# Performance work log

Hardware: AMD Instinct MI355X
Metric: run time of the kernel (lower is better)

## Reference

```python
import jax, jax.numpy as jnp
import numpy as np

N_NODES = 50000
N_EDGES = 800000
NODE_IN = 10
EDGE_IN = 7
H = 128
N_LAYERS = 6
OUT_DIM = 3


def setup_inputs() -> dict:
    key = jax.random.key(0)
    ks = jax.random.split(key, 32)
    s = 0.05
    inp = {
        "x": jax.random.normal(ks[0], (N_NODES, NODE_IN), jnp.float32),
        "edge_attr": jax.random.normal(ks[1], (N_EDGES, EDGE_IN), jnp.float32),
        "edge_index": jax.random.randint(ks[2], (2, N_EDGES), 0, N_NODES, jnp.int32),
        "bc_disp": jax.random.uniform(ks[3], (N_NODES, 1), jnp.float32),
        "bc_rot": jax.random.uniform(ks[4], (N_NODES, 1), jnp.float32),
        # node encoder: MLP(10, [H], H)
        "ne_w1": jax.random.normal(ks[5], (NODE_IN, H), jnp.float32) * s,
        "ne_b1": jnp.zeros((H,), jnp.float32),
        "ne_w2": jax.random.normal(ks[6], (H, H), jnp.float32) * s,
        "ne_b2": jnp.zeros((H,), jnp.float32),
        # edge encoder: MLP(7, [H], H)
        "ee_w1": jax.random.normal(ks[7], (EDGE_IN, H), jnp.float32) * s,
        "ee_b1": jnp.zeros((H,), jnp.float32),
        "ee_w2": jax.random.normal(ks[8], (H, H), jnp.float32) * s,
        "ee_b2": jnp.zeros((H,), jnp.float32),
        # 6 GraphNetworkLayers: edge model (3H -> H), node model (2H -> H)
        "mp_ew": jax.random.normal(ks[9], (N_LAYERS, 3 * H, H), jnp.float32) * s,
        "mp_eb": jnp.zeros((N_LAYERS, H), jnp.float32),
        "mp_nw": jax.random.normal(ks[10], (N_LAYERS, 2 * H, H), jnp.float32) * s,
        "mp_nb": jnp.zeros((N_LAYERS, H), jnp.float32),
        "d_w1": jax.random.normal(ks[11], (H, H), jnp.float32) * s,
        "d_b1": jnp.zeros((H,), jnp.float32),
        "d_w2": jax.random.normal(ks[12], (H, 64), jnp.float32) * s,
        "d_b2": jnp.zeros((64,), jnp.float32),
        "d_w3": jax.random.normal(ks[13], (64, OUT_DIM), jnp.float32) * (s * 5.0),
        "d_b3": jnp.full((OUT_DIM,), 0.5, jnp.float32),
    }
    return inp


def reference(x, edge_attr, edge_index, bc_disp, bc_rot,
              ne_w1, ne_b1, ne_w2, ne_b2,
              ee_w1, ee_b1, ee_w2, ee_b2,
              mp_ew, mp_eb, mp_nw, mp_nb,
              d_w1, d_b1, d_w2, d_b2, d_w3, d_b3):
    # encode nodes and edges (Linear -> ReLU -> Linear)
    h = jax.nn.relu(x @ ne_w1 + ne_b1) @ ne_w2 + ne_b2            # [N, H]
    e = jax.nn.relu(edge_attr @ ee_w1 + ee_b1) @ ee_w2 + ee_b2    # [E, H]
    src = edge_index[0]
    dst = edge_index[1]
    # 6 residual message-passing layers: gather -> edge MLP -> scatter-add -> node MLP
    for l in range(N_LAYERS):
        msg_in = jnp.concatenate([h[src], h[dst], e], axis=-1)    # [E, 3H]
        msg = jax.nn.relu(msg_in @ mp_ew[l] + mp_eb[l])           # [E, H]
        agg = jax.ops.segment_sum(msg, dst, num_segments=N_NODES)  # [N, H] (aggr='add')
        upd = jax.nn.relu(jnp.concatenate([h, agg], axis=-1) @ mp_nw[l] + mp_nb[l])
        h = h + upd                                               # residual
    # decode: Linear -> ReLU -> Linear -> ReLU -> Linear
    z = jax.nn.relu(h @ d_w1 + d_b1)
    z = jax.nn.relu(z @ d_w2 + d_b2)
    pred = z @ d_w3 + d_b3                                        # [N, 3]
    # hard boundary conditions
    pred = jnp.concatenate([pred[:, 0:2] * (1.0 - bc_disp),
                            pred[:, 2:3] * (1.0 - bc_rot)], axis=-1)
    return pred
```

## Files before the change

### kernel.cpp

```cpp
#include <hip/hip_runtime.h>
#include <hip/hip_bf16.h>

#define NN 50000
#define NE 800000
#define H 128

typedef __hip_bfloat16 bf16;
typedef __attribute__((ext_vector_type(8))) short short8v;
typedef __attribute__((ext_vector_type(4))) float f32x4;

static __device__ __forceinline__ unsigned short f2bf_bits(float x) {
  union { __hip_bfloat16 b; unsigned short u; } cv;
  cv.b = __float2bfloat16(x);
  return cv.u;
}

__global__ __launch_bounds__(256) void zero_counts_kernel(int* __restrict__ counts) {
  int i = blockIdx.x * 256 + threadIdx.x;
  if (i < NN) counts[i] = 0;
}

__global__ __launch_bounds__(256) void hist_kernel(const int* __restrict__ dstI,
                                                   int* __restrict__ counts) {
  int e = blockIdx.x * 256 + threadIdx.x;
  if (e < NE) atomicAdd(&counts[dstI[e]], 1);
}

__global__ __launch_bounds__(256) void scan_kernel(const int* __restrict__ counts,
                                                   int* __restrict__ cursor) {
  __shared__ int sdata[256];
  __shared__ int sbase;
  const int t = threadIdx.x;
  if (t == 0) sbase = 0;
  __syncthreads();
  for (int c0 = 0; c0 < NN; c0 += 256) {
    int i = c0 + t;
    int v = (i < NN) ? counts[i] : 0;
    sdata[t] = v;
    __syncthreads();
    #pragma unroll
    for (int off = 1; off < 256; off <<= 1) {
      int x = (t >= off) ? sdata[t - off] : 0;
      __syncthreads();
      sdata[t] += x;
      __syncthreads();
    }
    if (i < NN) cursor[i] = sbase + sdata[t] - v;
    __syncthreads();
    if (t == 255) sbase += sdata[255];
    __syncthreads();
  }
}

__global__ __launch_bounds__(256) void scatter_kernel(
    const float* __restrict__ ea, const int* __restrict__ srcI, const int* __restrict__ dstI,
    int* __restrict__ cursor, bf16* __restrict__ eap,
    int* __restrict__ srcp, int* __restrict__ dstp) {
  int e = blockIdx.x * 256 + threadIdx.x;
  if (e >= NE) return;
  int d = dstI[e];
  int pos = atomicAdd(&cursor[d], 1);
  srcp[pos] = srcI[e];
  dstp[pos] = d;
  #pragma unroll
  for (int k = 0; k < 7; ++k) eap[(size_t)pos * 7 + k] = __float2bfloat16(ea[(size_t)e * 7 + k]);
}

__global__ __launch_bounds__(256) void fuse_w3_kernel(
    const float* __restrict__ ee_w2, const float* __restrict__ ee_b2,
    const float* __restrict__ mp_ew, const float* __restrict__ mp_eb,
    float* __restrict__ W3p, float* __restrict__ c3)
{
  const int l = blockIdx.x >> 3;
  const int cc = (blockIdx.x & 7) * 16;
  __shared__ float sA[H * H];
  __shared__ float sB[H * 16];
  const float* W3 = mp_ew + (size_t)l * 384 * H + 256 * H;
  for (int i = threadIdx.x; i < H * H; i += 256) sA[i] = ee_w2[i];
  for (int i = threadIdx.x; i < H * 16; i += 256) {
    int k = i >> 4, j = i & 15;
    sB[i] = W3[k * H + cc + j];
  }
  __syncthreads();
  float* out = W3p + (size_t)l * H * H;
  for (int i = threadIdx.x; i < H * 16; i += 256) {
    int r = i >> 4, j = i & 15;
    float acc = 0.f;
    #pragma unroll 8
    for (int k = 0; k < H; ++k) acc += sA[r * H + k] * sB[k * 16 + j];
    out[r * H + cc + j] = acc;
  }
  if (threadIdx.x < 16) {
    int j = threadIdx.x;
    float acc = mp_eb[l * H + cc + j];
    for (int k = 0; k < H; ++k) acc += ee_b2[k] * sB[k * 16 + j];
    c3[l * H + cc + j] = acc;
  }
}

__global__ __launch_bounds__(256) void repack_w_kernel(
    const float* __restrict__ src0, size_t lstride, bf16* __restrict__ dst0, int K)
{
  const int l = blockIdx.x;
  const float* src = src0 + (size_t)l * lstride;
  bf16* dst = dst0 + (size_t)l * K * 128;
  const int nkk = K / 32;
  const int nslots = 8 * nkk * 64;
  for (int idx = threadIdx.x; idx < nslots; idx += 256) {
    int ng = idx / (nkk * 64);
    int rem = idx % (nkk * 64);
    int kk = rem / 64, ln = rem % 64;
    #pragma unroll
    for (int j = 0; j < 8; ++j) {
      int k = kk * 32 + ((ln >> 4) * 8) + j;
      int col = ng * 16 + (ln & 15);
      dst[(size_t)idx * 8 + j] = __float2bfloat16(src[(size_t)k * 128 + col]);
    }
  }
}

__global__ __launch_bounds__(256) void node_encoder_kernel(
    const float* __restrict__ in,
    const float* __restrict__ w1, const float* __restrict__ b1,
    const float* __restrict__ w2, const float* __restrict__ b2,
    float* __restrict__ out, int nrows)
{
  __shared__ float sw1[10 * H];
  __shared__ float sw2[H * H];
  __shared__ float sb1[H];
  __shared__ float sb2[H];
  __shared__ float sin_[8][10];
  __shared__ float st[8][H];

  for (int i = threadIdx.x; i < 10 * H; i += 256) sw1[i] = w1[i];
  for (int i = threadIdx.x; i < H * H; i += 256) sw2[i] = w2[i];
  if (threadIdx.x < H) { sb1[threadIdx.x] = b1[threadIdx.x]; sb2[threadIdx.x] = b2[threadIdx.x]; }
  __syncthreads();

  const int c = threadIdx.x & 127;
  const int hf = threadIdx.x >> 7;

  for (long long r0 = (long long)blockIdx.x * 8; r0 < nrows; r0 += (long long)gridDim.x * 8) {
    if (threadIdx.x < 80) {
      int j = threadIdx.x / 10, k = threadIdx.x % 10;
      long long r = r0 + j;
      sin_[j][k] = (r < nrows) ? in[r * 10 + k] : 0.f;
    }
    __syncthreads();
    #pragma unroll
    for (int t = 0; t < 4; ++t) {
      int idx = threadIdx.x + t * 256;
      int j = idx >> 7, k = idx & 127;
      float acc = sb1[k];
      #pragma unroll
      for (int i = 0; i < 10; ++i) acc += sin_[j][i] * sw1[i * H + k];
      st[j][k] = fmaxf(acc, 0.f);
    }
    __syncthreads();
    float a0 = sb2[c], a1 = a0, a2 = a0, a3 = a0;
    #pragma unroll 4
    for (int k4 = 0; k4 < H; k4 += 4) {
      float w0 = sw2[(k4 + 0) * H + c];
      float w1v = sw2[(k4 + 1) * H + c];
      float w2v = sw2[(k4 + 2) * H + c];
      float w3v = sw2[(k4 + 3) * H + c];
      float4 s0 = *(const float4*)&st[hf * 4 + 0][k4];
      float4 s1 = *(const float4*)&st[hf * 4 + 1][k4];
      float4 s2 = *(const float4*)&st[hf * 4 + 2][k4];
      float4 s3 = *(const float4*)&st[hf * 4 + 3][k4];
      a0 += s0.x * w0 + s0.y * w1v + s0.z * w2v + s0.w * w3v;
      a1 += s1.x * w0 + s1.y * w1v + s1.z * w2v + s1.w * w3v;
      a2 += s2.x * w0 + s2.y * w1v + s2.z * w2v + s2.w * w3v;
      a3 += s3.x * w0 + s3.y * w1v + s3.z * w2v + s3.w * w3v;
    }
    float accs[4] = {a0, a1, a2, a3};
    #pragma unroll
    for (int j = 0; j < 4; ++j) {
      long long r = r0 + hf * 4 + j;
      if (r < nrows) out[r * H + c] = accs[j];
    }
    __syncthreads();
  }
}

__global__ __launch_bounds__(512) void node_AB_kernel(
    const float* __restrict__ h, const float* __restrict__ W1f, const float* __restrict__ W2f,
    bf16* __restrict__ A, bf16* __restrict__ B, float* __restrict__ agg, int nrows)
{
  __shared__ float sw1[H * H];
  __shared__ float sw2[H * H];
  __shared__ float sh[16][H];
  for (int i = threadIdx.x; i < H * H; i += 512) { sw1[i] = W1f[i]; sw2[i] = W2f[i]; }
  __syncthreads();
  const int c = threadIdx.x & 127;
  const int q = threadIdx.x >> 7;
  for (long long r0 = (long long)blockIdx.x * 16; r0 < nrows; r0 += (long long)gridDim.x * 16) {
    #pragma unroll
    for (int t = 0; t < 4; ++t) {
      int idx = threadIdx.x + t * 512;
      int j = idx >> 7, k = idx & 127;
      long long r = r0 + j;
      sh[j][k] = (r < nrows) ? h[r * H + k] : 0.f;
    }
    __syncthreads();
    float aA[4] = {0, 0, 0, 0}, aB[4] = {0, 0, 0, 0};
    #pragma unroll 2
    for (int k4 = 0; k4 < H; k4 += 4) {
      float w10 = sw1[(k4 + 0) * H + c], w11 = sw1[(k4 + 1) * H + c];
      float w12 = sw1[(k4 + 2) * H + c], w13 = sw1[(k4 + 3) * H + c];
      float w20 = sw2[(k4 + 0) * H + c], w21 = sw2[(k4 + 1) * H + c];
      float w22 = sw2[(k4 + 2) * H + c], w23 = sw2[(k4 + 3) * H + c];
      #pragma unroll
      for (int j = 0; j < 4; ++j) {
        float4 s = *(const float4*)&sh[q * 4 + j][k4];
        aA[j] += s.x * w10 + s.y * w11 + s.z * w12 + s.w * w13;
        aB[j] += s.x * w20 + s.y * w21 + s.z * w22 + s.w * w23;
      }
    }
    #pragma unroll
    for (int j = 0; j < 4; ++j) {
      long long r = r0 + q * 4 + j;
      if (r < nrows) {
        A[r * H + c] = __float2bfloat16(aA[j]);
        B[r * H + c] = __float2bfloat16(aB[j]);
        agg[r * H + c] = 0.f;
      }
    }
    __syncthreads();
  }
}

__global__ __launch_bounds__(512) void edge_mfma_scatter(
    const bf16* __restrict__ eap,
    const int* __restrict__ srcp, const int* __restrict__ dstp,
    const bf16* __restrict__ A, const bf16* __restrict__ B,
    const float* __restrict__ ew1, const float* __restrict__ eb1,
    const bf16* __restrict__ W3b, const float* __restrict__ c3,
    float* __restrict__ agg, int nE)
{
  __shared__ unsigned short seaP[64][40];
  __shared__ int didx[64];
  __shared__ unsigned int shid[64 * 64];
  __shared__ bf16 sAld[64][136];

  const int t = threadIdx.x;
  const int lane = t & 63;
  const int wid = t >> 6;
  const int hm = wid >> 2;
  const int colbase = (wid & 3) * 32;

  for (int i = t; i < 64 * 40; i += 512) ((unsigned short*)seaP)[i] = 0;

  short8v bfrag[2][4];
  float c3v[2];
  #pragma unroll
  for (int n = 0; n < 2; ++n) {
    c3v[n] = c3[colbase + n * 16 + (lane & 15)];
    int ng = (colbase >> 4) + n;
    #pragma unroll
    for (int kk = 0; kk < 4; ++kk) {
      const bf16* p = W3b + ((size_t)(ng * 4 + kk) * 64 + lane) * 8;
      bfrag[n][kk] = *(const short8v*)p;
    }
  }
  short8v bew[2];
  float eb1v[2];
  #pragma unroll
  for (int n = 0; n < 2; ++n) {
    int col = colbase + n * 16 + (lane & 15);
    eb1v[n] = eb1[col];
    #pragma unroll
    for (int j = 0; j < 8; ++j) {
      int k = (lane >> 4) * 8 + j;
      bew[n][j] = (short)((k < 7) ? f2bf_bits(ew1[k * H + col]) : 0);
    }
  }
  __syncthreads();

  const long long stride = (long long)gridDim.x * 64;
  const int elA0 = t >> 4;
  const int elA1 = 32 + (t >> 4);
  const int segA = (t & 15) * 8;

  unsigned short pf_ea = 0;
  int     pf_d = 0;
  short8v pf_A0, pf_A1;
  long long e0 = (long long)blockIdx.x * 64;
  if (e0 < nE) {
    if (t < 448) pf_ea = ((const unsigned short*)eap)[e0 * 7 + t];
    if (t < 64)  pf_d = dstp[e0 + t];
    int s0 = srcp[e0 + elA0];
    pf_A0 = *(const short8v*)&A[(size_t)s0 * H + segA];
    int s1 = srcp[e0 + elA1];
    pf_A1 = *(const short8v*)&A[(size_t)s1 * H + segA];
  }

  for (; e0 < nE; e0 += stride) {
    if (t < 448) seaP[t / 7][t % 7] = pf_ea;
    if (t < 64)  didx[t] = pf_d;
    *(short8v*)&sAld[elA0][segA] = pf_A0;
    *(short8v*)&sAld[elA1][segA] = pf_A1;
    __syncthreads();

    long long e1 = e0 + stride;
    if (e1 < nE) {
      if (t < 448) pf_ea = ((const unsigned short*)eap)[e1 * 7 + t];
      if (t < 64)  pf_d = dstp[e1 + t];
      int s0 = srcp[e1 + elA0];
      pf_A0 = *(const short8v*)&A[(size_t)s0 * H + segA];
      int s1 = srcp[e1 + elA1];
      pf_A1 = *(const short8v*)&A[(size_t)s1 * H + segA];
    }

    {
      f32x4 h1[2][2];
      const f32x4 z = {0.f, 0.f, 0.f, 0.f};
      h1[0][0] = z; h1[0][1] = z; h1[1][0] = z; h1[1][1] = z;
      #pragma unroll
      for (int m = 0; m < 2; ++m) {
        int row = hm * 32 + m * 16 + (lane & 15);
        short8v afrag = *(const short8v*)((const char*)seaP + row * 80 + (lane >> 4) * 16);
        h1[m][0] = __builtin_amdgcn_mfma_f32_16x16x32_bf16(afrag, bew[0], h1[m][0], 0, 0, 0);
        h1[m][1] = __builtin_amdgcn_mfma_f32_16x16x32_bf16(afrag, bew[1], h1[m][1], 0, 0, 0);
      }
      #pragma unroll
      for (int m = 0; m < 2; ++m) {
        #pragma unroll
        for (int r = 0; r < 4; ++r) {
          int row = hm * 32 + m * 16 + (lane >> 4) * 4 + r;
          #pragma unroll
          for (int n = 0; n < 2; ++n) {
            int col = colbase + n * 16 + (lane & 15);
            float v = fmaxf(h1[m][n][r] + eb1v[n], 0.f);
            int off = (row * 256 + col * 2) ^ ((row & 7) << 4);
            *(unsigned short*)((char*)shid + off) = f2bf_bits(v);
          }
        }
      }
    }
    __syncthreads();

    f32x4 acc[2][2];
    const f32x4 z = {0.f, 0.f, 0.f, 0.f};
    acc[0][0] = z; acc[0][1] = z; acc[1][0] = z; acc[1][1] = z;
    #pragma unroll
    for (int m = 0; m < 2; ++m) {
      #pragma unroll
      for (int kk = 0; kk < 4; ++kk) {
        int row = hm * 32 + m * 16 + (lane & 15);
        int off = (row * 256 + kk * 64 + (lane >> 4) * 16) ^ ((row & 7) << 4);
        short8v afrag = *(const short8v*)((const char*)shid + off);
        acc[m][0] = __builtin_amdgcn_mfma_f32_16x16x32_bf16(afrag, bfrag[0][kk], acc[m][0], 0, 0, 0);
        acc[m][1] = __builtin_amdgcn_mfma_f32_16x16x32_bf16(afrag, bfrag[1][kk], acc[m][1], 0, 0, 0);
      }
    }

    const int col0 = colbase + (lane & 15);
    const int col1 = col0 + 16;
    #pragma unroll
    for (int m = 0; m < 2; ++m) {
      float vs0 = 0.f, vs1 = 0.f;
      float b0 = 0.f, b1 = 0.f;
      int dprev = -1;
      #pragma unroll
      for (int r = 0; r < 4; ++r) {
        int el = hm * 32 + m * 16 + (lane >> 4) * 4 + r;
        int d = didx[el];
        if (d != dprev) {
          if (dprev >= 0) {
            atomicAdd(&agg[(size_t)dprev * H + col0], vs0);
            atomicAdd(&agg[(size_t)dprev * H + col1], vs1);
          }
          vs0 = 0.f; vs1 = 0.f;
          b0 = __bfloat162float(B[(size_t)d * H + col0]);
          b1 = __bfloat162float(B[(size_t)d * H + col1]);
          dprev = d;
        }
        float a0v = __bfloat162float(sAld[el][col0]);
        float a1v = __bfloat162float(sAld[el][col1]);
        vs0 += fmaxf(acc[m][0][r] + c3v[0] + a0v + b0, 0.f);
        vs1 += fmaxf(acc[m][1][r] + c3v[1] + a1v + b1, 0.f);
      }
      atomicAdd(&agg[(size_t)dprev * H + col0], vs0);
      atomicAdd(&agg[(size_t)dprev * H + col1], vs1);
    }
    __syncthreads();
  }
}

template<int DO_AB>
__global__ __launch_bounds__(256) void fused_update_kernel(
    float* __restrict__ h, const float* __restrict__ aggin,
    const bf16* __restrict__ Wnb, const float* __restrict__ nb,
    const bf16* __restrict__ W1b, const bf16* __restrict__ W2b,
    bf16* __restrict__ A, bf16* __restrict__ B, float* __restrict__ aggz,
    int nrows)
{
  __shared__ unsigned int sKw[32 * 128];
  unsigned short* shnew = (unsigned short*)sKw;

  const int t = threadIdx.x;
  const int lane = t & 63;
  const int wid = t >> 6;
  const int colbase = wid * 32;

  short8v bU[2][8];
  float nbv[2];
  #pragma unroll
  for (int n = 0; n < 2; ++n) {
    int ng = wid * 2 + n;
    nbv[n] = nb[colbase + n * 16 + (lane & 15)];
    #pragma unroll
    for (int kk = 0; kk < 8; ++kk)
      bU[n][kk] = *(const short8v*)(Wnb + ((size_t)(ng * 8 + kk) * 64 + lane) * 8);
  }

  const int ntiles = (nrows + 31) / 32;
  for (int tile = blockIdx.x; tile < ntiles; tile += gridDim.x) {
    const int r0 = tile * 32;
    #pragma unroll
    for (int i = 0; i < 16; ++i) {
      int w = t + i * 256;
      int row = w >> 7, k2 = w & 127;
      int r = r0 + row;
      float v0 = 0.f, v1 = 0.f;
      if (r < nrows) {
        if (k2 < 64) { float2 p = *(const float2*)&h[(size_t)r * H + 2 * k2]; v0 = p.x; v1 = p.y; }
        else         { float2 p = *(const float2*)&aggin[(size_t)r * H + 2 * k2 - 128]; v0 = p.x; v1 = p.y; }
      }
      unsigned int wrd = (unsigned int)f2bf_bits(v0) | ((unsigned int)f2bf_bits(v1) << 16);
      sKw[((w * 4) ^ ((row & 7) << 4)) >> 2] = wrd;
    }
    __syncthreads();

    f32x4 acc[2][2];
    const f32x4 z = {0.f, 0.f, 0.f, 0.f};
    acc[0][0] = z; acc[0][1] = z; acc[1][0] = z; acc[1][1] = z;
    #pragma unroll
    for (int kk = 0; kk < 8; ++kk) {
      #pragma unroll
      for (int m = 0; m < 2; ++m) {
        int row = m * 16 + (lane & 15);
        int off = (row * 512 + kk * 64 + (lane >> 4) * 16) ^ ((row & 7) << 4);
        short8v afrag = *(const short8v*)((const char*)sKw + off);
        acc[m][0] = __builtin_amdgcn_mfma_f32_16x16x32_bf16(afrag, bU[0][kk], acc[m][0], 0, 0, 0);
        acc[m][1] = __builtin_amdgcn_mfma_f32_16x16x32_bf16(afrag, bU[1][kk], acc[m][1], 0, 0, 0);
      }
    }
    __syncthreads();

    #pragma unroll
    for (int m = 0; m < 2; ++m) {
      #pragma unroll
      for (int r = 0; r < 4; ++r) {
        int row = m * 16 + (lane >> 4) * 4 + r;
        int grow = r0 + row;
        #pragma unroll
        for (int n = 0; n < 2; ++n) {
          int col = colbase + n * 16 + (lane & 15);
          float u = fmaxf(acc[m][n][r] + nbv[n], 0.f);
          float hold = (grow < nrows) ? h[(size_t)grow * H + col] : 0.f;
          float hn = hold + u;
          if (grow < nrows) h[(size_t)grow * H + col] = hn;
          if (DO_AB) {
            int i16 = (row * 128 + col) ^ ((row & 7) << 3);
            shnew[i16] = f2bf_bits(hn);
          }
        }
      }
    }

    if (DO_AB) {
      __syncthreads();
      short8v bA[2][4], bB[2][4];
      #pragma unroll
      for (int n = 0; n < 2; ++n) {
        int ng = wid * 2 + n;
        #pragma unroll
        for (int kk = 0; kk < 4; ++kk) {
          bA[n][kk] = *(const short8v*)(W1b + ((size_t)(ng * 4 + kk) * 64 + lane) * 8);
          bB[n][kk] = *(const short8v*)(W2b + ((size_t)(ng * 4 + kk) * 64 + lane) * 8);
        }
      }
      f32x4 aA[2][2], aB2[2][2];
      aA[0][0] = z; aA[0][1] = z; aA[1][0] = z; aA[1][1] = z;
      aB2[0][0] = z; aB2[0][1] = z; aB2[1][0] = z; aB2[1][1] = z;
      #pragma unroll
      for (int kk = 0; kk < 4; ++kk) {
        #pragma unroll
        for (int m = 0; m < 2; ++m) {
          int row = m * 16 + (lane & 15);
          int off = (row * 256 + kk * 64 + (lane >> 4) * 16) ^ ((row & 7) << 4);
          short8v afrag = *(const short8v*)((const char*)shnew + off);
          aA[m][0] = __builtin_amdgcn_mfma_f32_16x16x32_bf16(afrag, bA[0][kk], aA[m][0], 0, 0, 0);
          aA[m][1] = __builtin_amdgcn_mfma_f32_16x16x32_bf16(afrag, bA[1][kk], aA[m][1], 0, 0, 0);
          aB2[m][0] = __builtin_amdgcn_mfma_f32_16x16x32_bf16(afrag, bB[0][kk], aB2[m][0], 0, 0, 0);
          aB2[m][1] = __builtin_amdgcn_mfma_f32_16x16x32_bf16(afrag, bB[1][kk], aB2[m][1], 0, 0, 0);
        }
      }
      #pragma unroll
      for (int m = 0; m < 2; ++m) {
        #pragma unroll
        for (int r = 0; r < 4; ++r) {
          int row = m * 16 + (lane >> 4) * 4 + r;
          int grow = r0 + row;
          if (grow < nrows) {
            #pragma unroll
            for (int n = 0; n < 2; ++n) {
              int col = colbase + n * 16 + (lane & 15);
              A[(size_t)grow * H + col] = __float2bfloat16(aA[m][n][r]);
              B[(size_t)grow * H + col] = __float2bfloat16(aB2[m][n][r]);
              aggz[(size_t)grow * H + col] = 0.f;
            }
          }
        }
      }
    }
    __syncthreads();
  }
}

__global__ __launch_bounds__(512) void decoder_kernel(
    const float* __restrict__ h,
    const float* __restrict__ w1, const float* __restrict__ b1,
    const float* __restrict__ w2, const float* __restrict__ b2,
    const float* __restrict__ w3, const float* __restrict__ b3,
    const float* __restrict__ bcd, const float* __restrict__ bcr,
    float* __restrict__ out, int nrows)
{
  __shared__ float sw1[H * H];
  __shared__ float sw2[H * 64];
  __shared__ float sw3[64 * 3];
  __shared__ float sb1[H], sb2[64], sb3[3];
  __shared__ float sh[16][H], st1[16][H], st2[16][64];
  for (int i = threadIdx.x; i < H * H; i += 512) sw1[i] = w1[i];
  for (int i = threadIdx.x; i < H * 64; i += 512) sw2[i] = w2[i];
  if (threadIdx.x < 64 * 3) sw3[threadIdx.x] = w3[threadIdx.x];
  if (threadIdx.x < H) sb1[threadIdx.x] = b1[threadIdx.x];
  if (threadIdx.x < 64) sb2[threadIdx.x] = b2[threadIdx.x];
  if (threadIdx.x < 3) sb3[threadIdx.x] = b3[threadIdx.x];
  __syncthreads();
  for (long long r0 = (long long)blockIdx.x * 16; r0 < nrows; r0 += (long long)gridDim.x * 16) {
    #pragma unroll
    for (int t = 0; t < 4; ++t) {
      int idx = threadIdx.x + t * 512;
      int j = idx >> 7, k = idx & 127;
      long long r = r0 + j;
      sh[j][k] = (r < nrows) ? h[r * H + k] : 0.f;
    }
    __syncthreads();
    #pragma unroll
    for (int t = 0; t < 4; ++t) {
      int idx = threadIdx.x + t * 512;
      int j = idx >> 7, k = idx & 127;
      float acc = sb1[k];
      #pragma unroll 8
      for (int i = 0; i < H; ++i) acc += sh[j][i] * sw1[i * H + k];
      st1[j][k] = fmaxf(acc, 0.f);
    }
    __syncthreads();
    #pragma unroll
    for (int t = 0; t < 2; ++t) {
      int idx = threadIdx.x + t * 512;
      int j = idx >> 6, k = idx & 63;
      float acc = sb2[k];
      #pragma unroll 8
      for (int i = 0; i < H; ++i) acc += st1[j][i] * sw2[i * 64 + k];
      st2[j][k] = fmaxf(acc, 0.f);
    }
    __syncthreads();
    if (threadIdx.x < 48) {
      int j = threadIdx.x / 3, o = threadIdx.x % 3;
      float acc = sb3[o];
      #pragma unroll 8
      for (int i = 0; i < 64; ++i) acc += st2[j][i] * sw3[i * 3 + o];
      long long r = r0 + j;
      if (r < nrows) {
        float m = (o < 2) ? (1.f - bcd[r]) : (1.f - bcr[r]);
        out[r * 3 + o] = acc * m;
      }
    }
    __syncthreads();
  }
}

extern "C" void kernel_launch(void* const* d_in, const int* in_sizes, int n_in,
                              void* d_out, int out_size, void* d_ws, size_t ws_size,
                              hipStream_t stream) {
  const float* x     = (const float*)d_in[0];
  const float* ea    = (const float*)d_in[1];
  const int*   eidx  = (const int*)d_in[2];
  const float* bcd   = (const float*)d_in[3];
  const float* bcr   = (const float*)d_in[4];
  const float* ne_w1 = (const float*)d_in[5];
  const float* ne_b1 = (const float*)d_in[6];
  const float* ne_w2 = (const float*)d_in[7];
  const float* ne_b2 = (const float*)d_in[8];
  const float* ee_w1 = (const float*)d_in[9];
  const float* ee_b1 = (const float*)d_in[10];
  const float* ee_w2 = (const float*)d_in[11];
  const float* ee_b2 = (const float*)d_in[12];
  const float* mp_ew = (const float*)d_in[13];
  const float* mp_eb = (const float*)d_in[14];
  const float* mp_nw = (const float*)d_in[15];
  const float* mp_nb = (const float*)d_in[16];
  const float* d_w1  = (const float*)d_in[17];
  const float* d_b1  = (const float*)d_in[18];
  const float* d_w2  = (const float*)d_in[19];
  const float* d_b2  = (const float*)d_in[20];
  const float* d_w3  = (const float*)d_in[21];
  const float* d_b3  = (const float*)d_in[22];

  const int* srcI = eidx;
  const int* dstI = eidx + NE;

  char* wsp = (char*)d_ws;
  float* h    = (float*)wsp; wsp += (size_t)NN * H * 4;
  float* agg  = (float*)wsp; wsp += (size_t)NN * H * 4;
  bf16*  A    = (bf16*)wsp;  wsp += (size_t)NN * H * 2;
  bf16*  B    = (bf16*)wsp;  wsp += (size_t)NN * H * 2;
  bf16*  eap  = (bf16*)wsp;  wsp += (size_t)NE * 7 * 2;
  int*   srcp = (int*)wsp;   wsp += (size_t)NE * 4;
  int*   dstp = (int*)wsp;   wsp += (size_t)NE * 4;
  bf16*  W3b  = (bf16*)wsp;  wsp += (size_t)6 * H * H * 2;
  bf16*  Wnb  = (bf16*)wsp;  wsp += (size_t)6 * 256 * H * 2;
  bf16*  W1b  = (bf16*)wsp;  wsp += (size_t)6 * H * H * 2;
  bf16*  W2b  = (bf16*)wsp;  wsp += (size_t)6 * H * H * 2;
  float* c3   = (float*)wsp; wsp += (size_t)6 * H * 4;
  int*   counts = (int*)A;
  int*   cursor = (int*)A + NN;
  float* W3p    = agg;

  zero_counts_kernel<<<(NN + 255) / 256, 256, 0, stream>>>(counts);
  hist_kernel<<<(NE + 255) / 256, 256, 0, stream>>>(dstI, counts);
  scan_kernel<<<1, 256, 0, stream>>>(counts, cursor);
  scatter_kernel<<<(NE + 255) / 256, 256, 0, stream>>>(ea, srcI, dstI, cursor, eap, srcp, dstp);

  fuse_w3_kernel<<<48, 256, 0, stream>>>(ee_w2, ee_b2, mp_ew, mp_eb, W3p, c3);
  repack_w_kernel<<<6, 256, 0, stream>>>(W3p, (size_t)H * H, W3b, 128);
  repack_w_kernel<<<6, 256, 0, stream>>>(mp_nw, (size_t)256 * H, Wnb, 256);
  repack_w_kernel<<<6, 256, 0, stream>>>(mp_ew, (size_t)384 * H, W1b, 128);
  repack_w_kernel<<<6, 256, 0, stream>>>(mp_ew + 128 * H, (size_t)384 * H, W2b, 128);

  node_encoder_kernel<<<2048, 256, 0, stream>>>(x, ne_w1, ne_b1, ne_w2, ne_b2, h, NN);
  node_AB_kernel<<<1024, 512, 0, stream>>>(h, mp_ew, mp_ew + 128 * H, A, B, agg, NN);

  for (int l = 0; l < 6; ++l) {
    edge_mfma_scatter<<<6250, 512, 0, stream>>>(eap, srcp, dstp, A, B, ee_w1, ee_b1,
                                                W3b + (size_t)l * H * H, c3 + l * H, agg, NE);
    if (l < 5) {
      fused_update_kernel<1><<<1563, 256, 0, stream>>>(
          h, agg, Wnb + (size_t)l * 256 * H, mp_nb + l * H,
          W1b + (size_t)(l + 1) * H * H, W2b + (size_t)(l + 1) * H * H,
          A, B, agg, NN);
    } else {
      fused_update_kernel<0><<<1563, 256, 0, stream>>>(
          h, agg, Wnb + (size_t)l * 256 * H, mp_nb + l * H,
          nullptr, nullptr, nullptr, nullptr, nullptr, NN);
    }
  }

  decoder_kernel<<<1024, 512, 0, stream>>>(h, d_w1, d_b1, d_w2, d_b2, d_w3, d_b3,
                                           bcd, bcr, (float*)d_out, NN);
}
```

Measured before the change: 2.810 ms.

## Assign destination segments to owning blocks and replace the serial scan

The edge kernel now gives each 64-edge block ownership of the destination segments that start within its range, extending into the next 64 edges to finish a boundary segment. It accumulates up to 16 owned destinations in shared memory and writes them to agg with plain stores, replacing most global float atomics; any further destinations still use atomics. The single-block prefix scan becomes a three-kernel block scan. The risks are extra passes that recompute the edge MLP for tail edges, a grid twice as large, lost cross-iteration prefetch, and correctness that depends on sorted dst order and on segments not spanning more than the next block.

New measurement: 3.038 ms. +8.1%, slower.

```diff
diff --git a/kernel.cpp b/kernel.cpp
--- a/kernel.cpp
+++ b/kernel.cpp
@@ -4,6 +4,7 @@
 #define NN 50000
 #define NE 800000
 #define H 128
+#define NBLK 196
 
 typedef __hip_bfloat16 bf16;
 typedef __attribute__((ext_vector_type(8))) short short8v;
@@ -26,30 +27,52 @@
   if (e < NE) atomicAdd(&counts[dstI[e]], 1);
 }
 
-__global__ __launch_bounds__(256) void scan_kernel(const int* __restrict__ counts,
-                                                   int* __restrict__ cursor) {
+__global__ __launch_bounds__(256) void scan1_kernel(const int* __restrict__ counts,
+                                                    int* __restrict__ bsum) {
   __shared__ int sdata[256];
-  __shared__ int sbase;
+  int i = blockIdx.x * 256 + threadIdx.x;
+  sdata[threadIdx.x] = (i < NN) ? counts[i] : 0;
+  __syncthreads();
+  for (int off = 128; off > 0; off >>= 1) {
+    if (threadIdx.x < off) sdata[threadIdx.x] += sdata[threadIdx.x + off];
+    __syncthreads();
+  }
+  if (threadIdx.x == 0) bsum[blockIdx.x] = sdata[0];
+}
+
+__global__ __launch_bounds__(256) void scan2_kernel(int* __restrict__ bsum) {
+  __shared__ int sdata[256];
   const int t = threadIdx.x;
-  if (t == 0) sbase = 0;
-  __syncthreads();
-  for (int c0 = 0; c0 < NN; c0 += 256) {
-    int i = c0 + t;
-    int v = (i < NN) ? counts[i] : 0;
-    sdata[t] = v;
-    __syncthreads();
-    #pragma unroll
-    for (int off = 1; off < 256; off <<= 1) {
-      int x = (t >= off) ? sdata[t - off] : 0;
-      __syncthreads();
-      sdata[t] += x;
-      __syncthreads();
-    }
-    if (i < NN) cursor[i] = sbase + sdata[t] - v;
-    __syncthreads();
-    if (t == 255) sbase += sdata[255];
-    __syncthreads();
-  }
+  int v = (t < NBLK) ? bsum[t] : 0;
+  sdata[t] = v;
+  __syncthreads();
+  #pragma unroll
+  for (int off = 1; off < 256; off <<= 1) {
+    int x = (t >= off) ? sdata[t - off] : 0;
+    __syncthreads();
+    sdata[t] += x;
+    __syncthreads();
+  }
+  if (t < NBLK) bsum[t] = sdata[t] - v;
+}
+
+__global__ __launch_bounds__(256) void scan3_kernel(const int* __restrict__ counts,
+                                                    const int* __restrict__ bsum,
+                                                    int* __restrict__ cursor) {
+  __shared__ int sdata[256];
+  const int t = threadIdx.x;
+  int i = blockIdx.x * 256 + t;
+  int v = (i < NN) ? counts[i] : 0;
+  sdata[t] = v;
+  __syncthreads();
+  #pragma unroll
+  for (int off = 1; off < 256; off <<= 1) {
+    int x = (t >= off) ? sdata[t - off] : 0;
+    __syncthreads();
+    sdata[t] += x;
+    __syncthreads();
+  }
+  if (i < NN) cursor[i] = bsum[blockIdx.x] + sdata[t] - v;
 }
 
 __global__ __launch_bounds__(256) void scatter_kernel(
@@ -230,7 +253,7 @@
   }
 }
 
-__global__ __launch_bounds__(512) void edge_mfma_scatter(
+__global__ __launch_bounds__(512) void edge_mfma_own(
     const bf16* __restrict__ eap,
     const int* __restrict__ srcp, const int* __restrict__ dstp,
     const bf16* __restrict__ A, const bf16* __restrict__ B,
@@ -238,18 +261,30 @@
     const bf16* __restrict__ W3b, const float* __restrict__ c3,
     float* __restrict__ agg, int nE)
 {
+  __shared__ int sdidx[129];
+  __shared__ int sssrc[128];
+  __shared__ unsigned long long sb[2];
+  __shared__ int sgdst[64];
   __shared__ unsigned short seaP[64][40];
-  __shared__ int didx[64];
   __shared__ unsigned int shid[64 * 64];
   __shared__ bf16 sAld[64][136];
+  __shared__ float sagg[16 * 128];
 
   const int t = threadIdx.x;
   const int lane = t & 63;
   const int wid = t >> 6;
   const int hm = wid >> 2;
   const int colbase = (wid & 3) * 32;
+  const long long L = (long long)blockIdx.x * 64;
 
   for (int i = t; i < 64 * 40; i += 512) ((unsigned short*)seaP)[i] = 0;
+  for (int i = t; i < 16 * 128; i += 512) sagg[i] = 0.f;
+  if (t < 128) {
+    long long s = L + t;
+    sdidx[1 + t] = (s < nE) ? dstp[s] : -1;
+    sssrc[t] = (s < nE) ? srcp[s] : 0;
+  }
+  if (t == 128) sdidx[0] = (L > 0) ? dstp[L - 1] : -1;
 
   short8v bfrag[2][4];
   float c3v[2];
@@ -258,10 +293,8 @@
     c3v[n] = c3[colbase + n * 16 + (lane & 15)];
     int ng = (colbase >> 4) + n;
     #pragma unroll
-    for (int kk = 0; kk < 4; ++kk) {
-      const bf16* p = W3b + ((size_t)(ng * 4 + kk) * 64 + lane) * 8;
-      bfrag[n][kk] = *(const short8v*)p;
-    }
+    for (int kk = 0; kk < 4; ++kk)
+      bfrag[n][kk] = *(const short8v*)(W3b + ((size_t)(ng * 4 + kk) * 64 + lane) * 8);
   }
   short8v bew[2];
   float eb1v[2];
@@ -277,40 +310,60 @@
   }
   __syncthreads();
 
-  const long long stride = (long long)gridDim.x * 64;
+  if (wid == 0) {
+    int j = lane;
+    bool bnd = sdidx[1 + j] != sdidx[j];
+    unsigned long long m = __ballot(bnd);
+    if (bnd) sgdst[(int)__popcll(m & ((2ull << j) - 1ull)) - 1] = sdidx[1 + j];
+    if (lane == 0) sb[0] = m;
+  } else if (wid == 1) {
+    int j = 64 + lane;
+    bool bnd = sdidx[1 + j] != sdidx[j];
+    unsigned long long m = __ballot(bnd);
+    if (lane == 0) sb[1] = m;
+  }
+  __syncthreads();
+  const unsigned long long b0 = sb[0], b1 = sb[1];
+  const int ndst = (int)__popcll(b0);
+
   const int elA0 = t >> 4;
   const int elA1 = 32 + (t >> 4);
   const int segA = (t & 15) * 8;
-
-  unsigned short pf_ea = 0;
-  int     pf_d = 0;
-  short8v pf_A0, pf_A1;
-  long long e0 = (long long)blockIdx.x * 64;
-  if (e0 < nE) {
-    if (t < 448) pf_ea = ((const unsigned short*)eap)[e0 * 7 + t];
-    if (t < 64)  pf_d = dstp[e0 + t];
-    int s0 = srcp[e0 + elA0];
-    pf_A0 = *(const short8v*)&A[(size_t)s0 * H + segA];
-    int s1 = srcp[e0 + elA1];
-    pf_A1 = *(const short8v*)&A[(size_t)s1 * H + segA];
-  }
-
-  for (; e0 < nE; e0 += stride) {
-    if (t < 448) seaP[t / 7][t % 7] = pf_ea;
-    if (t < 64)  didx[t] = pf_d;
-    *(short8v*)&sAld[elA0][segA] = pf_A0;
-    *(short8v*)&sAld[elA1][segA] = pf_A1;
-    __syncthreads();
-
-    long long e1 = e0 + stride;
-    if (e1 < nE) {
-      if (t < 448) pf_ea = ((const unsigned short*)eap)[e1 * 7 + t];
-      if (t < 64)  pf_d = dstp[e1 + t];
-      int s0 = srcp[e1 + elA0];
-      pf_A0 = *(const short8v*)&A[(size_t)s0 * H + segA];
-      int s1 = srcp[e1 + elA1];
-      pf_A1 = *(const short8v*)&A[(size_t)s1 * H + segA];
-    }
+  const int col0 = colbase + (lane & 15);
+  const int col1 = col0 + 16;
+
+  #pragma unroll 1
+  for (int pass = 0; pass < 2; ++pass) {
+    if (pass == 1 && (((b1 & 1ull) != 0) || b0 == 0)) break;
+    const int base = pass * 64;
+
+    if (t < 448) {
+      int e = t / 7, k = t % 7;
+      int j = base + e;
+      bool own;
+      if (j < 64) own = (b0 & ((2ull << j) - 1ull)) != 0;
+      else        own = ((b1 & ((2ull << (j - 64)) - 1ull)) == 0) && (b0 != 0);
+      if (own) seaP[e][k] = ((const unsigned short*)eap)[(L + j) * 7 + k];
+    }
+    {
+      int e0i = elA0, j0 = base + e0i;
+      bool own0;
+      if (j0 < 64) own0 = (b0 & ((2ull << j0) - 1ull)) != 0;
+      else         own0 = ((b1 & ((2ull << (j0 - 64)) - 1ull)) == 0) && (b0 != 0);
+      if (own0) {
+        int s = sssrc[j0];
+        *(short8v*)&sAld[e0i][segA] = *(const short8v*)&A[(size_t)s * H + segA];
+      }
+      int e1i = elA1, j1 = base + e1i;
+      bool own1;
+      if (j1 < 64) own1 = (b0 & ((2ull << j1) - 1ull)) != 0;
+      else         own1 = ((b1 & ((2ull << (j1 - 64)) - 1ull)) == 0) && (b0 != 0);
+      if (own1) {
+        int s = sssrc[j1];
+        *(short8v*)&sAld[e1i][segA] = *(const short8v*)&A[(size_t)s * H + segA];
+      }
+    }
+    __syncthreads();
 
     {
       f32x4 h1[2][2];
@@ -355,36 +408,71 @@
       }
     }
 
-    const int col0 = colbase + (lane & 15);
-    const int col1 = col0 + 16;
-    #pragma unroll
-    for (int m = 0; m < 2; ++m) {
-      float vs0 = 0.f, vs1 = 0.f;
-      float b0 = 0.f, b1 = 0.f;
-      int dprev = -1;
-      #pragma unroll
-      for (int r = 0; r < 4; ++r) {
-        int el = hm * 32 + m * 16 + (lane >> 4) * 4 + r;
-        int d = didx[el];
-        if (d != dprev) {
-          if (dprev >= 0) {
-            atomicAdd(&agg[(size_t)dprev * H + col0], vs0);
-            atomicAdd(&agg[(size_t)dprev * H + col1], vs1);
+    {
+      float vs0 = 0.f, vs1 = 0.f, bv0 = 0.f, bv1 = 0.f;
+      int liprev = -1, dprev = -1;
+      #pragma unroll
+      for (int m = 0; m < 2; ++m) {
+        #pragma unroll
+        for (int r = 0; r < 4; ++r) {
+          int el = hm * 32 + m * 16 + (lane >> 4) * 4 + r;
+          int j = base + el;
+          bool own;
+          int li;
+          if (j < 64) {
+            unsigned long long mk = b0 & ((2ull << j) - 1ull);
+            own = mk != 0;
+            li = (int)__popcll(mk) - 1;
+          } else {
+            own = ((b1 & ((2ull << (j - 64)) - 1ull)) == 0) && (b0 != 0);
+            li = ndst - 1;
           }
-          vs0 = 0.f; vs1 = 0.f;
-          b0 = __bfloat162float(B[(size_t)d * H + col0]);
-          b1 = __bfloat162float(B[(size_t)d * H + col1]);
-          dprev = d;
+          if (!own) li = -1;
+          if (li != liprev) {
+            if (liprev >= 0) {
+              if (liprev < 16) {
+                atomicAdd(&sagg[liprev * 128 + col0], vs0);
+                atomicAdd(&sagg[liprev * 128 + col1], vs1);
+              } else {
+                atomicAdd(&agg[(size_t)dprev * H + col0], vs0);
+                atomicAdd(&agg[(size_t)dprev * H + col1], vs1);
+              }
+            }
+            vs0 = 0.f; vs1 = 0.f;
+            liprev = li;
+            if (li >= 0) {
+              dprev = sdidx[1 + j];
+              bv0 = __bfloat162float(B[(size_t)dprev * H + col0]);
+              bv1 = __bfloat162float(B[(size_t)dprev * H + col1]);
+            }
+          }
+          if (li >= 0) {
+            float a0v = __bfloat162float(sAld[el][col0]);
+            float a1v = __bfloat162float(sAld[el][col1]);
+            vs0 += fmaxf(acc[m][0][r] + c3v[0] + a0v + bv0, 0.f);
+            vs1 += fmaxf(acc[m][1][r] + c3v[1] + a1v + bv1, 0.f);
+          }
         }
-        float a0v = __bfloat162float(sAld[el][col0]);
-        float a1v = __bfloat162float(sAld[el][col1]);
-        vs0 += fmaxf(acc[m][0][r] + c3v[0] + a0v + b0, 0.f);
-        vs1 += fmaxf(acc[m][1][r] + c3v[1] + a1v + b1, 0.f);
-      }
-      atomicAdd(&agg[(size_t)dprev * H + col0], vs0);
-      atomicAdd(&agg[(size_t)dprev * H + col1], vs1);
-    }
-    __syncthreads();
+      }
+      if (liprev >= 0) {
+        if (liprev < 16) {
+          atomicAdd(&sagg[liprev * 128 + col0], vs0);
+          atomicAdd(&sagg[liprev * 128 + col1], vs1);
+        } else {
+          atomicAdd(&agg[(size_t)dprev * H + col0], vs0);
+          atomicAdd(&agg[(size_t)dprev * H + col1], vs1);
+        }
+      }
+    }
+    __syncthreads();
+  }
+
+  {
+    int nli = ndst < 16 ? ndst : 16;
+    for (int i = t; i < nli * 128; i += 512) {
+      int li = i >> 7, col = i & 127;
+      agg[(size_t)sgdst[li] * H + col] = sagg[i];
+    }
   }
 }
 
@@ -627,13 +715,16 @@
   bf16*  W1b  = (bf16*)wsp;  wsp += (size_t)6 * H * H * 2;
   bf16*  W2b  = (bf16*)wsp;  wsp += (size_t)6 * H * H * 2;
   float* c3   = (float*)wsp; wsp += (size_t)6 * H * 4;
+  int*   bsum = (int*)wsp;   wsp += 256 * 4;
   int*   counts = (int*)A;
   int*   cursor = (int*)A + NN;
   float* W3p    = agg;
 
   zero_counts_kernel<<<(NN + 255) / 256, 256, 0, stream>>>(counts);
   hist_kernel<<<(NE + 255) / 256, 256, 0, stream>>>(dstI, counts);
-  scan_kernel<<<1, 256, 0, stream>>>(counts, cursor);
+  scan1_kernel<<<NBLK, 256, 0, stream>>>(counts, bsum);
+  scan2_kernel<<<1, 256, 0, stream>>>(bsum);
+  scan3_kernel<<<NBLK, 256, 0, stream>>>(counts, bsum, cursor);
   scatter_kernel<<<(NE + 255) / 256, 256, 0, stream>>>(ea, srcI, dstI, cursor, eap, srcp, dstp);
 
   fuse_w3_kernel<<<48, 256, 0, stream>>>(ee_w2, ee_b2, mp_ew, mp_eb, W3p, c3);
@@ -646,8 +737,8 @@
   node_AB_kernel<<<1024, 512, 0, stream>>>(h, mp_ew, mp_ew + 128 * H, A, B, agg, NN);
 
   for (int l = 0; l < 6; ++l) {
-    edge_mfma_scatter<<<6250, 512, 0, stream>>>(eap, srcp, dstp, A, B, ee_w1, ee_b1,
-                                                W3b + (size_t)l * H * H, c3 + l * H, agg, NE);
+    edge_mfma_own<<<12500, 512, 0, stream>>>(eap, srcp, dstp, A, B, ee_w1, ee_b1,
+                                             W3b + (size_t)l * H * H, c3 + l * H, agg, NE);
     if (l < 5) {
       fused_update_kernel<1><<<1563, 256, 0, stream>>>(
           h, agg, Wnb + (size_t)l * 256 * H, mp_nb + l * H,
```
